# Kernel tuning notes

Hardware: AMD Instinct MI355X
Metric: run time of the kernel (lower is better)

## Reference

```python
import jax, jax.numpy as jnp
import numpy as np

N_NODES = 100_000
N_EDGES = 2_500_000
HID = 32
SE3_NORM = 1.0 / np.sqrt(32.0)  # e3nn path normalization for 32x0e -> 32x0e


def setup_inputs() -> dict:
    key = jax.random.key(0)
    ks = jax.random.split(key, 14)
    inp = {
        "pos": jax.random.normal(ks[0], (N_NODES, 3), dtype=jnp.float32),
        "edge_index": jax.random.randint(ks[1], (2, N_EDGES), 0, N_NODES, dtype=jnp.int64),
        "Wl1": jax.random.normal(ks[2], (2, HID), dtype=jnp.float32) * 0.5,
        "bl1": jax.random.normal(ks[3], (HID,), dtype=jnp.float32) * 0.1,
        "Wr1": jax.random.normal(ks[4], (2, HID), dtype=jnp.float32) * 0.5,
        "Wl2": jax.random.normal(ks[5], (HID, HID), dtype=jnp.float32) * 0.15,
        "bl2": jax.random.normal(ks[6], (HID,), dtype=jnp.float32) * 0.1,
        "Wr2": jax.random.normal(ks[7], (HID, HID), dtype=jnp.float32) * 0.15,
        "Wse1": jax.random.normal(ks[8], (HID, HID), dtype=jnp.float32) * 0.15,
        "Wse2": jax.random.normal(ks[9], (HID, HID), dtype=jnp.float32) * 0.15,
        "W3": jax.random.normal(ks[10], (HID, HID), dtype=jnp.float32) * 0.15,
        "b3": jax.random.normal(ks[11], (HID,), dtype=jnp.float32) * 0.1,
        "W4": jax.random.normal(ks[12], (HID, 1), dtype=jnp.float32) * 0.15,
        "b4": jax.random.normal(ks[13], (1,), dtype=jnp.float32) * 0.1,
        "alpha": jnp.float32(0.5),
    }
    return inp


def _sage_conv(x, src, dst, Wl, bl, Wr, n_nodes):
    # gather messages from source nodes, scatter-sum onto destination nodes
    agg = jax.ops.segment_sum(x[src], dst, num_segments=n_nodes)  # [N, d_in]
    return agg @ Wl + bl + x @ Wr  # lin_l(agg) + lin_r(x); lin_r has no bias


def reference(pos, edge_index, Wl1, bl1, Wr1, Wl2, bl2, Wr2, Wse1, Wse2, W3, b3, W4, b4, alpha):
    n = pos.shape[0]
    x = pos[:, :2]                       # [N, 2]
    src, dst = edge_index[0], edge_index[1]

    h1 = _sage_conv(x, src, dst, Wl1, bl1, Wr1, n)   # [N, 32]
    h1 = jax.nn.leaky_relu(h1, negative_slope=0.01)  # dropout = identity (eval)
    h1 = (h1 @ Wse1) * SE3_NORM                      # SE3Linear 32x0e->32x0e

    h2 = _sage_conv(h1, src, dst, Wl2, bl2, Wr2, n)
    h2 = jax.nn.leaky_relu(h2, negative_slope=0.01)
    h2 = (h2 @ Wse2) * SE3_NORM

    x_skip = alpha * h1 + h2
    x_out = jax.nn.relu(x_skip @ W3 + b3)            # mlp3 (dropout identity)
    pred = x_out @ W4 + b4                           # mlp4
    return pred.squeeze(-1)                          # [N]
```

## Files before the change

kernel.cpp:

```cpp
#include <hip/hip_runtime.h>
#include <hip/hip_fp16.h>

#define HID 32
#define LEAKY 0.01f
#define SE3NORM 0.17677669529663687f
#define SCAN_TILE 1024
#define NBK 128
#define GA 256
#define NPB2 64


__global__ void k_bhist(const int* __restrict__ ei, int* __restrict__ bh,
                        int E, int B1, int chunk) {
    extern __shared__ int lh[];
    int g = blockIdx.x;
    for (int i = threadIdx.x; i < B1; i += 256) lh[i] = 0;
    __syncthreads();
    int beg = g * chunk, end = min(E, beg + chunk);
    for (int e = beg + (int)threadIdx.x; e < end; e += 256)
        atomicAdd(&lh[ei[E + e] >> 7], 1);
    __syncthreads();
    for (int b = threadIdx.x; b < B1; b += 256) bh[b * GA + g] = lh[b];
}

__global__ void k_scan1(int* __restrict__ data, int* __restrict__ bsum, int M) {
    __shared__ int lds[256];
    int t = threadIdx.x;
    int base = blockIdx.x * SCAN_TILE + t * 4;
    int v0 = (base + 0 < M) ? data[base + 0] : 0;
    int v1 = (base + 1 < M) ? data[base + 1] : 0;
    int v2 = (base + 2 < M) ? data[base + 2] : 0;
    int v3 = (base + 3 < M) ? data[base + 3] : 0;
    int s = v0 + v1 + v2 + v3;
    lds[t] = s;
    __syncthreads();
    for (int off = 1; off < 256; off <<= 1) {
        int x = (t >= off) ? lds[t - off] : 0;
        __syncthreads();
        lds[t] += x;
        __syncthreads();
    }
    int ex = lds[t] - s;
    if (base + 0 < M) data[base + 0] = ex;
    if (base + 1 < M) data[base + 1] = ex + v0;
    if (base + 2 < M) data[base + 2] = ex + v0 + v1;
    if (base + 3 < M) data[base + 3] = ex + v0 + v1 + v2;
    if (t == 255) bsum[blockIdx.x] = lds[255];
}

__global__ void k_scan2(int* __restrict__ bsum, int B) {
    __shared__ int lds[256];
    int t = threadIdx.x;
    int v = (t < B) ? bsum[t] : 0;
    lds[t] = v;
    __syncthreads();
    for (int off = 1; off < 256; off <<= 1) {
        int x = (t >= off) ? lds[t - off] : 0;
        __syncthreads();
        lds[t] += x;
        __syncthreads();
    }
    if (t < B) bsum[t] = lds[t] - v;
}

__global__ void k_scan3(int* __restrict__ data, const int* __restrict__ bsum,
                        int* __restrict__ cursor, int M, int N) {
    int i = blockIdx.x * blockDim.x + threadIdx.x;
    if (i >= M) return;
    int off = data[i] + bsum[i / SCAN_TILE];
    data[i] = off;
    if (cursor && i < N) cursor[i] = off;
}

__global__ void k_bscatter(const int* __restrict__ ei, const int* __restrict__ bh,
                           int* __restrict__ bucketed, int E, int B1, int chunk) {
    extern __shared__ int cur[];
    int g = blockIdx.x;
    for (int b = threadIdx.x; b < B1; b += 256) cur[b] = bh[b * GA + g];
    __syncthreads();
    int beg = g * chunk, end = min(E, beg + chunk);
    for (int e = beg + (int)threadIdx.x; e < end; e += 256) {
        int d = ei[E + e];
        int s = ei[e];
        int b = d >> 7;
        int p = atomicAdd(&cur[b], 1);
        bucketed[p] = s | ((d & (NBK - 1)) << 24);
    }
}

__global__ void k_bsort(const int* __restrict__ bh, const int* __restrict__ bucketed,
                        int* __restrict__ sorted_src, int* __restrict__ offsets,
                        int E, int N, int B1) {
    __shared__ int hist[NBK], sc[NBK], base[NBK];
    int b = blockIdx.x;
    int t = threadIdx.x;
    int bs = bh[b * GA];
    int be = (b == B1 - 1) ? E : bh[(b + 1) * GA];
    if (t < NBK) hist[t] = 0;
    __syncthreads();
    for (int e = bs + t; e < be; e += 256)
        atomicAdd(&hist[bucketed[e] >> 24], 1);
    __syncthreads();
    int v = (t < NBK) ? hist[t] : 0;
    if (t < NBK) sc[t] = v;
    __syncthreads();
    for (int off = 1; off < NBK; off <<= 1) {
        int x = (t < NBK && t >= off) ? sc[t - off] : 0;
        __syncthreads();
        if (t < NBK) sc[t] += x;
        __syncthreads();
    }
    if (t < NBK) base[t] = sc[t] - v;
    __syncthreads();
    if (t < NBK) hist[t] = base[t];
    __syncthreads();
    for (int e = bs + t; e < be; e += 256) {
        int pv = bucketed[e];
        int p = atomicAdd(&hist[pv >> 24], 1);
        sorted_src[bs + p] = pv & 0x00FFFFFF;
    }
    int node = b * NBK + t;
    if (t < NBK && node < N) offsets[node] = bs + base[t];
    if (b == B1 - 1 && t == 0) offsets[N] = E;
}

__global__ void k_hist_rank(const int* __restrict__ ei, int* __restrict__ hist,
                            int* __restrict__ rank, int E) {
    int base = (blockIdx.x * blockDim.x + threadIdx.x) * 4;
#pragma unroll
    for (int u = 0; u < 4; u++) {
        int e = base + u;
        if (e < E) rank[e] = atomicAdd(&hist[ei[E + e]], 1);
    }
}
__global__ void k_hist(const int* __restrict__ ei, int* __restrict__ hist, int E) {
    int base = (blockIdx.x * blockDim.x + threadIdx.x) * 4;
#pragma unroll
    for (int u = 0; u < 4; u++) {
        int e = base + u;
        if (e < E) atomicAdd(&hist[ei[E + e]], 1);
    }
}
__global__ void k_scatter_rank(const int* __restrict__ ei, const int* __restrict__ offsets,
                               const int* __restrict__ rank, int* __restrict__ sorted_src, int E) {
    int base = (blockIdx.x * blockDim.x + threadIdx.x) * 4;
#pragma unroll
    for (int u = 0; u < 4; u++) {
        int e = base + u;
        if (e < E) sorted_src[offsets[ei[E + e]] + rank[e]] = ei[e];
    }
}
__global__ void k_scatter_atomic(const int* __restrict__ ei, int* __restrict__ cursor,
                                 int* __restrict__ sorted_src, int E) {
    int base = (blockIdx.x * blockDim.x + threadIdx.x) * 4;
#pragma unroll
    for (int u = 0; u < 4; u++) {
        int e = base + u;
        if (e < E) {
            int p = atomicAdd(&cursor[ei[E + e]], 1);
            sorted_src[p] = ei[e];
        }
    }
}

__global__ __launch_bounds__(256, 1) void k_node1(
                        const int* __restrict__ offsets, const int* __restrict__ sorted_src,
                        const float* __restrict__ pos,
                        const float* __restrict__ Wl1, const float* __restrict__ bl1,
                        const float* __restrict__ Wr1, const float* __restrict__ Wse1,
                        __half* __restrict__ h1out, int N) {
    __shared__ float sWl1[2 * HID], sWr1[2 * HID], sbl1[HID], sWse1[HID * HID];
    __shared__ float sH[32][HID + 1];
    for (int i = threadIdx.x; i < 2 * HID; i += blockDim.x) { sWl1[i] = Wl1[i]; sWr1[i] = Wr1[i]; }
    for (int i = threadIdx.x; i < HID; i += blockDim.x) sbl1[i] = bl1[i];
    for (int i = threadIdx.x; i < HID * HID; i += blockDim.x) sWse1[i] = Wse1[i];
    __syncthreads();

    const int lt = threadIdx.x;
    const int nodeL = lt >> 3;
    const int t = lt & 7;
    const int node = blockIdx.x * 32 + nodeL;
    const bool live = node < N;

    float a0 = 0.f, a1 = 0.f;
    if (live) {
        int beg = offsets[node], end = offsets[node + 1];
        for (int e = beg + t; e < end; e += 8) {
            int s = sorted_src[e];
            a0 += pos[s * 3];
            a1 += pos[s * 3 + 1];
        }
    }
    a0 += __shfl_xor(a0, 1); a1 += __shfl_xor(a1, 1);
    a0 += __shfl_xor(a0, 2); a1 += __shfl_xor(a1, 2);
    a0 += __shfl_xor(a0, 4); a1 += __shfl_xor(a1, 4);

    if (live) {
        float x0 = pos[3 * node], x1 = pos[3 * node + 1];
#pragma unroll
        for (int jj = 0; jj < 4; jj++) {
            int k = t * 4 + jj;
            float v = a0 * sWl1[k] + a1 * sWl1[HID + k] + sbl1[k] + x0 * sWr1[k] + x1 * sWr1[HID + k];
            sH[nodeL][k] = v > 0.f ? v : LEAKY * v;
        }
    }
    __syncthreads();

    if (live) {
        union Pack4 { __half h[4]; float2 v; };
        Pack4 p;
#pragma unroll
        for (int jj = 0; jj < 4; jj++) {
            int j = t * 4 + jj;
            float acc = 0.f;
#pragma unroll 8
            for (int k = 0; k < HID; k++) acc += sH[nodeL][k] * sWse1[k * HID + j];
            p.h[jj] = __float2half(acc * SE3NORM);
        }
        *(float2*)&h1out[(size_t)node * HID + t * 4] = p.v;
    }
}

__device__ __forceinline__ void acc_h1frag(float2 r, float4& acc) {
    __half2 p01 = __builtin_bit_cast(__half2, r.x);
    __half2 p23 = __builtin_bit_cast(__half2, r.y);
    acc.x += __low2float(p01); acc.y += __high2float(p01);
    acc.z += __low2float(p23); acc.w += __high2float(p23);
}

__global__ __launch_bounds__(512, 1) void k_node2out(
                           const int* __restrict__ offsets, const int* __restrict__ sorted_src,
                           const __half* __restrict__ h1,
                           const float* __restrict__ Wl2, const float* __restrict__ bl2,
                           const float* __restrict__ Wr2, const float* __restrict__ Wse2,
                           const float* __restrict__ W3, const float* __restrict__ b3,
                           const float* __restrict__ W4, const float* __restrict__ b4,
                           const float* __restrict__ alpha_p,
                           float* __restrict__ out, int N) {
    __shared__ float sWl2[HID * HID], sWr2[HID * HID], sWse2[HID * HID], sW3[HID * HID];
    __shared__ float sbl2[HID], sb3[HID], sW4[HID];
    __shared__ float sb4, salpha;
    __shared__ float sA[NPB2][HID + 1], sB[NPB2][HID + 1];
    for (int i = threadIdx.x; i < HID * HID; i += blockDim.x) {
        sWl2[i] = Wl2[i]; sWr2[i] = Wr2[i]; sWse2[i] = Wse2[i]; sW3[i] = W3[i];
    }
    for (int i = threadIdx.x; i < HID; i += blockDim.x) { sbl2[i] = bl2[i]; sb3[i] = b3[i]; sW4[i] = W4[i]; }
    if (threadIdx.x == 0) { sb4 = b4[0]; salpha = alpha_p[0]; }
    __syncthreads();

    const int lt = threadIdx.x;
    const int nodeL = lt >> 3;
    const int t = lt & 7;
    const int node = blockIdx.x * NPB2 + nodeL;
    const bool live = node < N;

    if (live) {
        float2 ro = *(const float2*)&h1[(size_t)node * HID + t * 4];

        int beg = offsets[node], end = offsets[node + 1];
        float4 acc = make_float4(0.f, 0.f, 0.f, 0.f);
        int e = beg;
        for (; e + 8 <= end; e += 8) {
            int s0 = sorted_src[e + 0], s1 = sorted_src[e + 1];
            int s2 = sorted_src[e + 2], s3 = sorted_src[e + 3];
            int s4 = sorted_src[e + 4], s5 = sorted_src[e + 5];
            int s6 = sorted_src[e + 6], s7 = sorted_src[e + 7];
            float2 r0 = *(const float2*)&h1[(size_t)s0 * HID + t * 4];
            float2 r1 = *(const float2*)&h1[(size_t)s1 * HID + t * 4];
            float2 r2 = *(const float2*)&h1[(size_t)s2 * HID + t * 4];
            float2 r3 = *(const float2*)&h1[(size_t)s3 * HID + t * 4];
            float2 r4 = *(const float2*)&h1[(size_t)s4 * HID + t * 4];
            float2 r5 = *(const float2*)&h1[(size_t)s5 * HID + t * 4];
            float2 r6 = *(const float2*)&h1[(size_t)s6 * HID + t * 4];
            float2 r7 = *(const float2*)&h1[(size_t)s7 * HID + t * 4];
            acc_h1frag(r0, acc); acc_h1frag(r1, acc);
            acc_h1frag(r2, acc); acc_h1frag(r3, acc);
            acc_h1frag(r4, acc); acc_h1frag(r5, acc);
            acc_h1frag(r6, acc); acc_h1frag(r7, acc);
        }
        for (; e + 4 <= end; e += 4) {
            int s0 = sorted_src[e + 0], s1 = sorted_src[e + 1];
            int s2 = sorted_src[e + 2], s3 = sorted_src[e + 3];
            float2 r0 = *(const float2*)&h1[(size_t)s0 * HID + t * 4];
            float2 r1 = *(const float2*)&h1[(size_t)s1 * HID + t * 4];
            float2 r2 = *(const float2*)&h1[(size_t)s2 * HID + t * 4];
            float2 r3 = *(const float2*)&h1[(size_t)s3 * HID + t * 4];
            acc_h1frag(r0, acc); acc_h1frag(r1, acc);
            acc_h1frag(r2, acc); acc_h1frag(r3, acc);
        }
        for (; e < end; e++) {
            int s = sorted_src[e];
            float2 r = *(const float2*)&h1[(size_t)s * HID + t * 4];
            acc_h1frag(r, acc);
        }
        __half2 o01 = __builtin_bit_cast(__half2, ro.x);
        __half2 o23 = __builtin_bit_cast(__half2, ro.y);
        sA[nodeL][t * 4 + 0] = acc.x; sA[nodeL][t * 4 + 1] = acc.y;
        sA[nodeL][t * 4 + 2] = acc.z; sA[nodeL][t * 4 + 3] = acc.w;
        sB[nodeL][t * 4 + 0] = __low2float(o01); sB[nodeL][t * 4 + 1] = __high2float(o01);
        sB[nodeL][t * 4 + 2] = __low2float(o23); sB[nodeL][t * 4 + 3] = __high2float(o23);
    }
    __syncthreads();

    float h2r[4];
    if (live) {
#pragma unroll
        for (int jj = 0; jj < 4; jj++) {
            int j = t * 4 + jj;
            float acc = sbl2[j];
#pragma unroll 8
            for (int k = 0; k < HID; k++)
                acc += sA[nodeL][k] * sWl2[k * HID + j] + sB[nodeL][k] * sWr2[k * HID + j];
            h2r[jj] = acc > 0.f ? acc : LEAKY * acc;
        }
    }
    __syncthreads();
    if (live) {
#pragma unroll
        for (int jj = 0; jj < 4; jj++) sA[nodeL][t * 4 + jj] = h2r[jj];
    }
    __syncthreads();

    if (live) {
#pragma unroll
        for (int jj = 0; jj < 4; jj++) {
            int j = t * 4 + jj;
            float acc = 0.f;
#pragma unroll 8
            for (int k = 0; k < HID; k++) acc += sA[nodeL][k] * sWse2[k * HID + j];
            sB[nodeL][j] = salpha * sB[nodeL][j] + acc * SE3NORM;
        }
    }
    __syncthreads();

    float part = 0.f;
#pragma unroll
    for (int jj = 0; jj < 4; jj++) {
        int j = t * 4 + jj;
        float acc = sb3[j];
        if (live) {
#pragma unroll 8
            for (int k = 0; k < HID; k++) acc += sB[nodeL][k] * sW3[k * HID + j];
        }
        part += (acc > 0.f ? acc : 0.f) * sW4[j];
    }
    part += __shfl_xor(part, 1);
    part += __shfl_xor(part, 2);
    part += __shfl_xor(part, 4);
    if (live && t == 0) out[node] = part + sb4;
}

extern "C" void kernel_launch(void* const* d_in, const int* in_sizes, int n_in,
                              void* d_out, int out_size, void* d_ws, size_t ws_size,
                              hipStream_t stream) {
    const float* pos  = (const float*)d_in[0];
    const int*   ei   = (const int*)d_in[1];
    const float* Wl1  = (const float*)d_in[2];
    const float* bl1  = (const float*)d_in[3];
    const float* Wr1  = (const float*)d_in[4];
    const float* Wl2  = (const float*)d_in[5];
    const float* bl2  = (const float*)d_in[6];
    const float* Wr2  = (const float*)d_in[7];
    const float* Wse1 = (const float*)d_in[8];
    const float* Wse2 = (const float*)d_in[9];
    const float* W3   = (const float*)d_in[10];
    const float* b3   = (const float*)d_in[11];
    const float* W4   = (const float*)d_in[12];
    const float* b4   = (const float*)d_in[13];
    const float* alp  = (const float*)d_in[14];
    float* out = (float*)d_out;

    const int N = in_sizes[0] / 3;
    const int E = in_sizes[1] / 2;
    const int blk = 256;
    const size_t h1bytes = (size_t)N * HID * sizeof(__half);

    const int B1 = (N + NBK - 1) / NBK;
    const int M2 = B1 * GA;
    const int S2 = (M2 + SCAN_TILE - 1) / SCAN_TILE;
    {
        int* bh         = (int*)d_ws;
        int* bsum       = bh + M2;
        int* bucketed   = bsum + 256;
        int* sorted_src = bucketed + E;
        int* offsets    = sorted_src + E;
        uintptr_t hp = ((uintptr_t)(offsets + N + 1) + 15) & ~(uintptr_t)15;
        size_t need = (hp - (uintptr_t)d_ws) + h1bytes;
        if (need <= ws_size && S2 <= 256) {
            __half* h1 = (__half*)hp;
            const int chunk = (E + GA - 1) / GA;
            const size_t ldsB = (size_t)B1 * sizeof(int);
            k_bhist<<<GA, 256, ldsB, stream>>>(ei, bh, E, B1, chunk);
            k_scan1<<<S2, 256, 0, stream>>>(bh, bsum, M2);
            k_scan2<<<1, 256, 0, stream>>>(bsum, S2);
            k_scan3<<<(M2 + blk - 1) / blk, blk, 0, stream>>>(bh, bsum, nullptr, M2, 0);
            k_bscatter<<<GA, 256, ldsB, stream>>>(ei, bh, bucketed, E, B1, chunk);
            k_bsort<<<B1, 256, 0, stream>>>(bh, bucketed, sorted_src, offsets, E, N, B1);
            k_node1<<<(N + 31) / 32, 256, 0, stream>>>(offsets, sorted_src, pos,
                                                       Wl1, bl1, Wr1, Wse1, h1, N);
            k_node2out<<<(N + NPB2 - 1) / NPB2, 512, 0, stream>>>(offsets, sorted_src, h1,
                                                          Wl2, bl2, Wr2, Wse2,
                                                          W3, b3, W4, b4, alp, out, N);
            return;
        }
    }

    const int M = N + 1;
    const int B = (M + SCAN_TILE - 1) / SCAN_TILE;
    int* hist       = (int*)d_ws;
    int* offsets    = hist + M;
    int* bsum       = offsets + M;
    int* sorted_src = bsum + 256;
    int* aux        = sorted_src + E;
    uintptr_t hpA = ((uintptr_t)(aux + E) + 15) & ~(uintptr_t)15;
    uintptr_t hpB = ((uintptr_t)(aux + N) + 15) & ~(uintptr_t)15;
    size_t needA = (hpA - (uintptr_t)d_ws) + h1bytes;
    const bool useRank = (needA <= ws_size);
    __half* h1 = (__half*)(useRank ? hpA : hpB);

    hipMemsetAsync(hist, 0, (size_t)M * sizeof(int), stream);
    const int egrid4 = (E / 4 + blk) / blk;
    if (useRank) {
        k_hist_rank<<<egrid4, blk, 0, stream>>>(ei, hist, aux, E);
    } else {
        k_hist<<<egrid4, blk, 0, stream>>>(ei, hist, E);
    }
    k_scan1<<<B, 256, 0, stream>>>(hist, bsum, M);
    k_scan2<<<1, 256, 0, stream>>>(bsum, B);
    k_scan3<<<(M + blk - 1) / blk, blk, 0, stream>>>(hist, bsum, useRank ? nullptr : aux, M, N);
    int* offs = hist;
    if (useRank) {
        k_scatter_rank<<<egrid4, blk, 0, stream>>>(ei, offs, aux, sorted_src, E);
    } else {
        k_scatter_atomic<<<egrid4, blk, 0, stream>>>(ei, aux, sorted_src, E);
    }
    k_node1<<<(N + 31) / 32, 256, 0, stream>>>(offs, sorted_src, pos, Wl1, bl1, Wr1, Wse1, h1, N);
    k_node2out<<<(N + NPB2 - 1) / NPB2, 512, 0, stream>>>(offs, sorted_src, h1, Wl2, bl2, Wr2, Wse2,
                                                  W3, b3, W4, b4, alp, out, N);
}
```

Baseline: 258.8 us.

## Split h1 into two half-width planes and vectorize small matmuls with float4

Stores the fp16 h1 features as two separate 16-channel planes (32 bytes per node each), so the layer-2 gather runs in two passes, each touching a smaller, more cache-friendly array. Each thread now loads 4 bytes per neighbour per pass instead of 8 bytes once. The per-node 32x32 matmuls are rewritten to read weights as float4 from LDS, with padding changed to HID+4 for alignment. The cost is reading the edge list twice and issuing twice as many gather instructions.

```diff
diff --git a/kernel.cpp b/kernel.cpp
--- a/kernel.cpp
+++ b/kernel.cpp
@@ -168,9 +168,9 @@
                         const float* __restrict__ pos,
                         const float* __restrict__ Wl1, const float* __restrict__ bl1,
                         const float* __restrict__ Wr1, const float* __restrict__ Wse1,
-                        __half* __restrict__ h1out, int N) {
+                        __half* __restrict__ h1a, __half* __restrict__ h1b, int N) {
     __shared__ float sWl1[2 * HID], sWr1[2 * HID], sbl1[HID], sWse1[HID * HID];
-    __shared__ float sH[32][HID + 1];
+    __shared__ float sH[32][HID + 4];
     for (int i = threadIdx.x; i < 2 * HID; i += blockDim.x) { sWl1[i] = Wl1[i]; sWr1[i] = Wr1[i]; }
     for (int i = threadIdx.x; i < HID; i += blockDim.x) sbl1[i] = bl1[i];
     for (int i = threadIdx.x; i < HID * HID; i += blockDim.x) sWse1[i] = Wse1[i];
@@ -207,30 +207,33 @@
     __syncthreads();
 
     if (live) {
+        float4 acc = make_float4(0.f, 0.f, 0.f, 0.f);
+#pragma unroll 8
+        for (int k = 0; k < HID; k++) {
+            float hk = sH[nodeL][k];
+            float4 w = *(const float4*)&sWse1[k * HID + t * 4];
+            acc.x += hk * w.x; acc.y += hk * w.y;
+            acc.z += hk * w.z; acc.w += hk * w.w;
+        }
         union Pack4 { __half h[4]; float2 v; };
         Pack4 p;
-#pragma unroll
-        for (int jj = 0; jj < 4; jj++) {
-            int j = t * 4 + jj;
-            float acc = 0.f;
-#pragma unroll 8
-            for (int k = 0; k < HID; k++) acc += sH[nodeL][k] * sWse1[k * HID + j];
-            p.h[jj] = __float2half(acc * SE3NORM);
-        }
-        *(float2*)&h1out[(size_t)node * HID + t * 4] = p.v;
-    }
-}
-
-__device__ __forceinline__ void acc_h1frag(float2 r, float4& acc) {
-    __half2 p01 = __builtin_bit_cast(__half2, r.x);
-    __half2 p23 = __builtin_bit_cast(__half2, r.y);
-    acc.x += __low2float(p01); acc.y += __high2float(p01);
-    acc.z += __low2float(p23); acc.w += __high2float(p23);
+        p.h[0] = __float2half(acc.x * SE3NORM);
+        p.h[1] = __float2half(acc.y * SE3NORM);
+        p.h[2] = __float2half(acc.z * SE3NORM);
+        p.h[3] = __float2half(acc.w * SE3NORM);
+        if (t < 4) *(float2*)&h1a[(size_t)node * 16 + t * 4] = p.v;
+        else       *(float2*)&h1b[(size_t)node * 16 + (t - 4) * 4] = p.v;
+    }
+}
+
+__device__ __forceinline__ void acc_pair(unsigned int r, float& x, float& y) {
+    __half2 p = __builtin_bit_cast(__half2, r);
+    x += __low2float(p); y += __high2float(p);
 }
 
 __global__ __launch_bounds__(512, 1) void k_node2out(
                            const int* __restrict__ offsets, const int* __restrict__ sorted_src,
-                           const __half* __restrict__ h1,
+                           const __half* __restrict__ h1a, const __half* __restrict__ h1b,
                            const float* __restrict__ Wl2, const float* __restrict__ bl2,
                            const float* __restrict__ Wr2, const float* __restrict__ Wse2,
                            const float* __restrict__ W3, const float* __restrict__ b3,
@@ -240,7 +243,7 @@
     __shared__ float sWl2[HID * HID], sWr2[HID * HID], sWse2[HID * HID], sW3[HID * HID];
     __shared__ float sbl2[HID], sb3[HID], sW4[HID];
     __shared__ float sb4, salpha;
-    __shared__ float sA[NPB2][HID + 1], sB[NPB2][HID + 1];
+    __shared__ float sA[NPB2][HID + 4], sB[NPB2][HID + 4];
     for (int i = threadIdx.x; i < HID * HID; i += blockDim.x) {
         sWl2[i] = Wl2[i]; sWr2[i] = Wr2[i]; sWse2[i] = Wse2[i]; sW3[i] = W3[i];
     }
@@ -255,95 +258,132 @@
     const bool live = node < N;
 
     if (live) {
-        float2 ro = *(const float2*)&h1[(size_t)node * HID + t * 4];
-
-        int beg = offsets[node], end = offsets[node + 1];
-        float4 acc = make_float4(0.f, 0.f, 0.f, 0.f);
+        const int beg = offsets[node], end = offsets[node + 1];
+        unsigned int oa = *(const unsigned int*)((const char*)h1a + ((size_t)node * 32 + t * 4));
+        unsigned int ob = *(const unsigned int*)((const char*)h1b + ((size_t)node * 32 + t * 4));
+
+        float a0 = 0.f, a1 = 0.f;
         int e = beg;
         for (; e + 8 <= end; e += 8) {
             int s0 = sorted_src[e + 0], s1 = sorted_src[e + 1];
             int s2 = sorted_src[e + 2], s3 = sorted_src[e + 3];
             int s4 = sorted_src[e + 4], s5 = sorted_src[e + 5];
             int s6 = sorted_src[e + 6], s7 = sorted_src[e + 7];
-            float2 r0 = *(const float2*)&h1[(size_t)s0 * HID + t * 4];
-            float2 r1 = *(const float2*)&h1[(size_t)s1 * HID + t * 4];
-            float2 r2 = *(const float2*)&h1[(size_t)s2 * HID + t * 4];
-            float2 r3 = *(const float2*)&h1[(size_t)s3 * HID + t * 4];
-            float2 r4 = *(const float2*)&h1[(size_t)s4 * HID + t * 4];
-            float2 r5 = *(const float2*)&h1[(size_t)s5 * HID + t * 4];
-            float2 r6 = *(const float2*)&h1[(size_t)s6 * HID + t * 4];
-            float2 r7 = *(const float2*)&h1[(size_t)s7 * HID + t * 4];
-            acc_h1frag(r0, acc); acc_h1frag(r1, acc);
-            acc_h1frag(r2, acc); acc_h1frag(r3, acc);
-            acc_h1frag(r4, acc); acc_h1frag(r5, acc);
-            acc_h1frag(r6, acc); acc_h1frag(r7, acc);
-        }
-        for (; e + 4 <= end; e += 4) {
+            unsigned int r0 = *(const unsigned int*)((const char*)h1a + ((size_t)s0 * 32 + t * 4));
+            unsigned int r1 = *(const unsigned int*)((const char*)h1a + ((size_t)s1 * 32 + t * 4));
+            unsigned int r2 = *(const unsigned int*)((const char*)h1a + ((size_t)s2 * 32 + t * 4));
+            unsigned int r3 = *(const unsigned int*)((const char*)h1a + ((size_t)s3 * 32 + t * 4));
+            unsigned int r4 = *(const unsigned int*)((const char*)h1a + ((size_t)s4 * 32 + t * 4));
+            unsigned int r5 = *(const unsigned int*)((const char*)h1a + ((size_t)s5 * 32 + t * 4));
+            unsigned int r6 = *(const unsigned int*)((const char*)h1a + ((size_t)s6 * 32 + t * 4));
+            unsigned int r7 = *(const unsigned int*)((const char*)h1a + ((size_t)s7 * 32 + t * 4));
+            acc_pair(r0, a0, a1); acc_pair(r1, a0, a1);
+            acc_pair(r2, a0, a1); acc_pair(r3, a0, a1);
+            acc_pair(r4, a0, a1); acc_pair(r5, a0, a1);
+            acc_pair(r6, a0, a1); acc_pair(r7, a0, a1);
+        }
+        for (; e < end; e++) {
+            int s = sorted_src[e];
+            unsigned int r = *(const unsigned int*)((const char*)h1a + ((size_t)s * 32 + t * 4));
+            acc_pair(r, a0, a1);
+        }
+        sA[nodeL][t * 2 + 0] = a0;
+        sA[nodeL][t * 2 + 1] = a1;
+
+        float b0 = 0.f, b1 = 0.f;
+        e = beg;
+        for (; e + 8 <= end; e += 8) {
             int s0 = sorted_src[e + 0], s1 = sorted_src[e + 1];
             int s2 = sorted_src[e + 2], s3 = sorted_src[e + 3];
-            float2 r0 = *(const float2*)&h1[(size_t)s0 * HID + t * 4];
-            float2 r1 = *(const float2*)&h1[(size_t)s1 * HID + t * 4];
-            float2 r2 = *(const float2*)&h1[(size_t)s2 * HID + t * 4];
-            float2 r3 = *(const float2*)&h1[(size_t)s3 * HID + t * 4];
-            acc_h1frag(r0, acc); acc_h1frag(r1, acc);
-            acc_h1frag(r2, acc); acc_h1frag(r3, acc);
+            int s4 = sorted_src[e + 4], s5 = sorted_src[e + 5];
+            int s6 = sorted_src[e + 6], s7 = sorted_src[e + 7];
+            unsigned int r0 = *(const unsigned int*)((const char*)h1b + ((size_t)s0 * 32 + t * 4));
+            unsigned int r1 = *(const unsigned int*)((const char*)h1b + ((size_t)s1 * 32 + t * 4));
+            unsigned int r2 = *(const unsigned int*)((const char*)h1b + ((size_t)s2 * 32 + t * 4));
+            unsigned int r3 = *(const unsigned int*)((const char*)h1b + ((size_t)s3 * 32 + t * 4));
+            unsigned int r4 = *(const unsigned int*)((const char*)h1b + ((size_t)s4 * 32 + t * 4));
+            unsigned int r5 = *(const unsigned int*)((const char*)h1b + ((size_t)s5 * 32 + t * 4));
+            unsigned int r6 = *(const unsigned int*)((const char*)h1b + ((size_t)s6 * 32 + t * 4));
+            unsigned int r7 = *(const unsigned int*)((const char*)h1b + ((size_t)s7 * 32 + t * 4));
+            acc_pair(r0, b0, b1); acc_pair(r1, b0, b1);
+            acc_pair(r2, b0, b1); acc_pair(r3, b0, b1);
+            acc_pair(r4, b0, b1); acc_pair(r5, b0, b1);
+            acc_pair(r6, b0, b1); acc_pair(r7, b0, b1);
         }
         for (; e < end; e++) {
             int s = sorted_src[e];
-            float2 r = *(const float2*)&h1[(size_t)s * HID + t * 4];
-            acc_h1frag(r, acc);
-        }
-        __half2 o01 = __builtin_bit_cast(__half2, ro.x);
-        __half2 o23 = __builtin_bit_cast(__half2, ro.y);
-        sA[nodeL][t * 4 + 0] = acc.x; sA[nodeL][t * 4 + 1] = acc.y;
-        sA[nodeL][t * 4 + 2] = acc.z; sA[nodeL][t * 4 + 3] = acc.w;
-        sB[nodeL][t * 4 + 0] = __low2float(o01); sB[nodeL][t * 4 + 1] = __high2float(o01);
-        sB[nodeL][t * 4 + 2] = __low2float(o23); sB[nodeL][t * 4 + 3] = __high2float(o23);
+            unsigned int r = *(const unsigned int*)((const char*)h1b + ((size_t)s * 32 + t * 4));
+            acc_pair(r, b0, b1);
+        }
+        sA[nodeL][16 + t * 2 + 0] = b0;
+        sA[nodeL][16 + t * 2 + 1] = b1;
+
+        __half2 pa = __builtin_bit_cast(__half2, oa);
+        __half2 pb = __builtin_bit_cast(__half2, ob);
+        sB[nodeL][t * 2 + 0]      = __low2float(pa); sB[nodeL][t * 2 + 1]      = __high2float(pa);
+        sB[nodeL][16 + t * 2 + 0] = __low2float(pb); sB[nodeL][16 + t * 2 + 1] = __high2float(pb);
     }
     __syncthreads();
 
     float h2r[4];
     if (live) {
-#pragma unroll
-        for (int jj = 0; jj < 4; jj++) {
-            int j = t * 4 + jj;
-            float acc = sbl2[j];
+        h2r[0] = sbl2[t * 4 + 0]; h2r[1] = sbl2[t * 4 + 1];
+        h2r[2] = sbl2[t * 4 + 2]; h2r[3] = sbl2[t * 4 + 3];
 #pragma unroll 8
-            for (int k = 0; k < HID; k++)
-                acc += sA[nodeL][k] * sWl2[k * HID + j] + sB[nodeL][k] * sWr2[k * HID + j];
-            h2r[jj] = acc > 0.f ? acc : LEAKY * acc;
-        }
-    }
-    __syncthreads();
-    if (live) {
-#pragma unroll
-        for (int jj = 0; jj < 4; jj++) sA[nodeL][t * 4 + jj] = h2r[jj];
-    }
-    __syncthreads();
-
-    if (live) {
-#pragma unroll
-        for (int jj = 0; jj < 4; jj++) {
-            int j = t * 4 + jj;
-            float acc = 0.f;
+        for (int k = 0; k < HID; k++) {
+            float a = sA[nodeL][k];
+            float b = sB[nodeL][k];
+            float4 wl = *(const float4*)&sWl2[k * HID + t * 4];
+            float4 wr = *(const float4*)&sWr2[k * HID + t * 4];
+            h2r[0] += a * wl.x + b * wr.x;
+            h2r[1] += a * wl.y + b * wr.y;
+            h2r[2] += a * wl.z + b * wr.z;
+            h2r[3] += a * wl.w + b * wr.w;
+        }
+#pragma unroll
+        for (int jj = 0; jj < 4; jj++) h2r[jj] = h2r[jj] > 0.f ? h2r[jj] : LEAKY * h2r[jj];
+    }
+    __syncthreads();
+    if (live) {
+        float4 st = make_float4(h2r[0], h2r[1], h2r[2], h2r[3]);
+        *(float4*)&sA[nodeL][t * 4] = st;
+    }
+    __syncthreads();
+
+    if (live) {
+        float4 acc = make_float4(0.f, 0.f, 0.f, 0.f);
 #pragma unroll 8
-            for (int k = 0; k < HID; k++) acc += sA[nodeL][k] * sWse2[k * HID + j];
-            sB[nodeL][j] = salpha * sB[nodeL][j] + acc * SE3NORM;
-        }
-    }
-    __syncthreads();
-
+        for (int k = 0; k < HID; k++) {
+            float a = sA[nodeL][k];
+            float4 w = *(const float4*)&sWse2[k * HID + t * 4];
+            acc.x += a * w.x; acc.y += a * w.y;
+            acc.z += a * w.z; acc.w += a * w.w;
+        }
+        float4 own = *(const float4*)&sB[nodeL][t * 4];
+        own.x = salpha * own.x + acc.x * SE3NORM;
+        own.y = salpha * own.y + acc.y * SE3NORM;
+        own.z = salpha * own.z + acc.z * SE3NORM;
+        own.w = salpha * own.w + acc.w * SE3NORM;
+        *(float4*)&sB[nodeL][t * 4] = own;
+    }
+    __syncthreads();
+
+    float acc4[4];
+    acc4[0] = sb3[t * 4 + 0]; acc4[1] = sb3[t * 4 + 1];
+    acc4[2] = sb3[t * 4 + 2]; acc4[3] = sb3[t * 4 + 3];
+    if (live) {
+#pragma unroll 8
+        for (int k = 0; k < HID; k++) {
+            float s = sB[nodeL][k];
+            float4 w = *(const float4*)&sW3[k * HID + t * 4];
+            acc4[0] += s * w.x; acc4[1] += s * w.y;
+            acc4[2] += s * w.z; acc4[3] += s * w.w;
+        }
+    }
     float part = 0.f;
 #pragma unroll
-    for (int jj = 0; jj < 4; jj++) {
-        int j = t * 4 + jj;
-        float acc = sb3[j];
-        if (live) {
-#pragma unroll 8
-            for (int k = 0; k < HID; k++) acc += sB[nodeL][k] * sW3[k * HID + j];
-        }
-        part += (acc > 0.f ? acc : 0.f) * sW4[j];
-    }
+    for (int jj = 0; jj < 4; jj++)
+        part += (acc4[jj] > 0.f ? acc4[jj] : 0.f) * sW4[t * 4 + jj];
     part += __shfl_xor(part, 1);
     part += __shfl_xor(part, 2);
     part += __shfl_xor(part, 4);
@@ -387,7 +427,8 @@
         uintptr_t hp = ((uintptr_t)(offsets + N + 1) + 15) & ~(uintptr_t)15;
         size_t need = (hp - (uintptr_t)d_ws) + h1bytes;
         if (need <= ws_size && S2 <= 256) {
-            __half* h1 = (__half*)hp;
+            __half* h1a = (__half*)hp;
+            __half* h1b = h1a + (size_t)N * 16;
             const int chunk = (E + GA - 1) / GA;
             const size_t ldsB = (size_t)B1 * sizeof(int);
             k_bhist<<<GA, 256, ldsB, stream>>>(ei, bh, E, B1, chunk);
@@ -397,8 +438,8 @@
             k_bscatter<<<GA, 256, ldsB, stream>>>(ei, bh, bucketed, E, B1, chunk);
             k_bsort<<<B1, 256, 0, stream>>>(bh, bucketed, sorted_src, offsets, E, N, B1);
             k_node1<<<(N + 31) / 32, 256, 0, stream>>>(offsets, sorted_src, pos,
-                                                       Wl1, bl1, Wr1, Wse1, h1, N);
-            k_node2out<<<(N + NPB2 - 1) / NPB2, 512, 0, stream>>>(offsets, sorted_src, h1,
+                                                       Wl1, bl1, Wr1, Wse1, h1a, h1b, N);
+            k_node2out<<<(N + NPB2 - 1) / NPB2, 512, 0, stream>>>(offsets, sorted_src, h1a, h1b,
                                                           Wl2, bl2, Wr2, Wse2,
                                                           W3, b3, W4, b4, alp, out, N);
             return;
@@ -416,7 +457,8 @@
     uintptr_t hpB = ((uintptr_t)(aux + N) + 15) & ~(uintptr_t)15;
     size_t needA = (hpA - (uintptr_t)d_ws) + h1bytes;
     const bool useRank = (needA <= ws_size);
-    __half* h1 = (__half*)(useRank ? hpA : hpB);
+    __half* h1a = (__half*)(useRank ? hpA : hpB);
+    __half* h1b = h1a + (size_t)N * 16;
 
     hipMemsetAsync(hist, 0, (size_t)M * sizeof(int), stream);
     const int egrid4 = (E / 4 + blk) / blk;
@@ -434,7 +476,7 @@
     } else {
         k_scatter_atomic<<<egrid4, blk, 0, stream>>>(ei, aux, sorted_src, E);
     }
-    k_node1<<<(N + 31) / 32, 256, 0, stream>>>(offs, sorted_src, pos, Wl1, bl1, Wr1, Wse1, h1, N);
-    k_node2out<<<(N + NPB2 - 1) / NPB2, 512, 0, stream>>>(offs, sorted_src, h1, Wl2, bl2, Wr2, Wse2,
+    k_node1<<<(N + 31) / 32, 256, 0, stream>>>(offs, sorted_src, pos, Wl1, bl1, Wr1, Wse1, h1a, h1b, N);
+    k_node2out<<<(N + NPB2 - 1) / NPB2, 512, 0, stream>>>(offs, sorted_src, h1a, h1b, Wl2, bl2, Wr2, Wse2,
                                                   W3, b3, W4, b4, alp, out, N);
 }
```

Measured after the change: 257.8 us. No clear change (-0.4%).

## Fuse bucket sort with layer-1 node computation and vectorize LDS matvecs

Applied to the files above, without the earlier changes.

Merges the per-bucket sort kernel with the first SAGE layer. While counting destination histograms, the block accumulates pos[src] x/y sums into shared atomics, then computes h1 for its 128 nodes in the same block. This removes one launch and the second pass over sorted_src. The change also adds nontemporal loads on edge streams, float4 weight reads from LDS with +4 padding in the matvecs, and drops the 4-wide tail loop. Float shared atomics make the summation order nondeterministic, and each block has only 128 destination nodes of work for layer 1.

```diff
diff --git a/kernel.cpp b/kernel.cpp
--- a/kernel.cpp
+++ b/kernel.cpp
@@ -18,7 +18,7 @@
     __syncthreads();
     int beg = g * chunk, end = min(E, beg + chunk);
     for (int e = beg + (int)threadIdx.x; e < end; e += 256)
-        atomicAdd(&lh[ei[E + e] >> 7], 1);
+        atomicAdd(&lh[__builtin_nontemporal_load(&ei[E + e]) >> 7], 1);
     __syncthreads();
     for (int b = threadIdx.x; b < B1; b += 256) bh[b * GA + g] = lh[b];
 }
@@ -80,26 +80,42 @@
     __syncthreads();
     int beg = g * chunk, end = min(E, beg + chunk);
     for (int e = beg + (int)threadIdx.x; e < end; e += 256) {
-        int d = ei[E + e];
-        int s = ei[e];
+        int d = __builtin_nontemporal_load(&ei[E + e]);
+        int s = __builtin_nontemporal_load(&ei[e]);
         int b = d >> 7;
         int p = atomicAdd(&cur[b], 1);
         bucketed[p] = s | ((d & (NBK - 1)) << 24);
     }
 }
 
-__global__ void k_bsort(const int* __restrict__ bh, const int* __restrict__ bucketed,
-                        int* __restrict__ sorted_src, int* __restrict__ offsets,
-                        int E, int N, int B1) {
+__global__ __launch_bounds__(256, 1) void k_bsort_node1(
+        const int* __restrict__ bh, const int* __restrict__ bucketed,
+        const float* __restrict__ pos,
+        const float* __restrict__ Wl1, const float* __restrict__ bl1,
+        const float* __restrict__ Wr1, const float* __restrict__ Wse1,
+        int* __restrict__ sorted_src, int* __restrict__ offsets,
+        __half* __restrict__ h1, int E, int N, int B1) {
     __shared__ int hist[NBK], sc[NBK], base[NBK];
-    int b = blockIdx.x;
-    int t = threadIdx.x;
-    int bs = bh[b * GA];
-    int be = (b == B1 - 1) ? E : bh[(b + 1) * GA];
-    if (t < NBK) hist[t] = 0;
-    __syncthreads();
-    for (int e = bs + t; e < be; e += 256)
-        atomicAdd(&hist[bucketed[e] >> 24], 1);
+    __shared__ float aggx[NBK], aggy[NBK];
+    __shared__ float sWl1[2 * HID], sWr1[2 * HID], sbl1[HID], sWse1[HID * HID];
+    __shared__ float sH[32][HID + 4];
+    const int b = blockIdx.x;
+    const int t = threadIdx.x;
+    for (int i = t; i < 2 * HID; i += 256) { sWl1[i] = Wl1[i]; sWr1[i] = Wr1[i]; }
+    for (int i = t; i < HID; i += 256) sbl1[i] = bl1[i];
+    for (int i = t; i < HID * HID; i += 256) sWse1[i] = Wse1[i];
+    const int bs = bh[b * GA];
+    const int be = (b == B1 - 1) ? E : bh[(b + 1) * GA];
+    if (t < NBK) { hist[t] = 0; aggx[t] = 0.f; aggy[t] = 0.f; }
+    __syncthreads();
+    for (int e = bs + t; e < be; e += 256) {
+        int pv = bucketed[e];
+        int dl = pv >> 24;
+        int s = pv & 0x00FFFFFF;
+        atomicAdd(&hist[dl], 1);
+        atomicAdd(&aggx[dl], pos[s * 3]);
+        atomicAdd(&aggy[dl], pos[s * 3 + 1]);
+    }
     __syncthreads();
     int v = (t < NBK) ? hist[t] : 0;
     if (t < NBK) sc[t] = v;
@@ -119,9 +135,46 @@
         int p = atomicAdd(&hist[pv >> 24], 1);
         sorted_src[bs + p] = pv & 0x00FFFFFF;
     }
-    int node = b * NBK + t;
-    if (t < NBK && node < N) offsets[node] = bs + base[t];
+    int nodeg = b * NBK + t;
+    if (t < NBK && nodeg < N) offsets[nodeg] = bs + base[t];
     if (b == B1 - 1 && t == 0) offsets[N] = E;
+    __syncthreads();
+    const int nodeL = t >> 3;
+    const int lane = t & 7;
+    for (int c = 0; c < NBK / 32; c++) {
+        const int dl = c * 32 + nodeL;
+        const int node = b * NBK + dl;
+        const bool live = node < N;
+        if (live) {
+            float a0 = aggx[dl], a1 = aggy[dl];
+            float x0 = pos[3 * node], x1 = pos[3 * node + 1];
+#pragma unroll
+            for (int jj = 0; jj < 4; jj++) {
+                int k = lane * 4 + jj;
+                float vv = a0 * sWl1[k] + a1 * sWl1[HID + k] + sbl1[k]
+                         + x0 * sWr1[k] + x1 * sWr1[HID + k];
+                sH[nodeL][k] = vv > 0.f ? vv : LEAKY * vv;
+            }
+        }
+        __syncthreads();
+        if (live) {
+            float4 acc = make_float4(0.f, 0.f, 0.f, 0.f);
+#pragma unroll 8
+            for (int k = 0; k < HID; k++) {
+                float hk = sH[nodeL][k];
+                float4 w = *(const float4*)&sWse1[k * HID + lane * 4];
+                acc.x += hk * w.x; acc.y += hk * w.y;
+                acc.z += hk * w.z; acc.w += hk * w.w;
+            }
+            union Pack4 { __half h[4]; float2 v; } p;
+            p.h[0] = __float2half(acc.x * SE3NORM);
+            p.h[1] = __float2half(acc.y * SE3NORM);
+            p.h[2] = __float2half(acc.z * SE3NORM);
+            p.h[3] = __float2half(acc.w * SE3NORM);
+            *(float2*)&h1[(size_t)node * HID + lane * 4] = p.v;
+        }
+        __syncthreads();
+    }
 }
 
 __global__ void k_hist_rank(const int* __restrict__ ei, int* __restrict__ hist,
@@ -168,9 +221,9 @@
                         const float* __restrict__ pos,
                         const float* __restrict__ Wl1, const float* __restrict__ bl1,
                         const float* __restrict__ Wr1, const float* __restrict__ Wse1,
-                        __half* __restrict__ h1out, int N) {
+                        __half* __restrict__ h1, int N) {
     __shared__ float sWl1[2 * HID], sWr1[2 * HID], sbl1[HID], sWse1[HID * HID];
-    __shared__ float sH[32][HID + 1];
+    __shared__ float sH[32][HID + 4];
     for (int i = threadIdx.x; i < 2 * HID; i += blockDim.x) { sWl1[i] = Wl1[i]; sWr1[i] = Wr1[i]; }
     for (int i = threadIdx.x; i < HID; i += blockDim.x) sbl1[i] = bl1[i];
     for (int i = threadIdx.x; i < HID * HID; i += blockDim.x) sWse1[i] = Wse1[i];
@@ -207,17 +260,20 @@
     __syncthreads();
 
     if (live) {
-        union Pack4 { __half h[4]; float2 v; };
-        Pack4 p;
-#pragma unroll
-        for (int jj = 0; jj < 4; jj++) {
-            int j = t * 4 + jj;
-            float acc = 0.f;
+        float4 acc = make_float4(0.f, 0.f, 0.f, 0.f);
 #pragma unroll 8
-            for (int k = 0; k < HID; k++) acc += sH[nodeL][k] * sWse1[k * HID + j];
-            p.h[jj] = __float2half(acc * SE3NORM);
-        }
-        *(float2*)&h1out[(size_t)node * HID + t * 4] = p.v;
+        for (int k = 0; k < HID; k++) {
+            float hk = sH[nodeL][k];
+            float4 w = *(const float4*)&sWse1[k * HID + t * 4];
+            acc.x += hk * w.x; acc.y += hk * w.y;
+            acc.z += hk * w.z; acc.w += hk * w.w;
+        }
+        union Pack4 { __half h[4]; float2 v; } p;
+        p.h[0] = __float2half(acc.x * SE3NORM);
+        p.h[1] = __float2half(acc.y * SE3NORM);
+        p.h[2] = __float2half(acc.z * SE3NORM);
+        p.h[3] = __float2half(acc.w * SE3NORM);
+        *(float2*)&h1[(size_t)node * HID + t * 4] = p.v;
     }
 }
 
@@ -240,7 +296,7 @@
     __shared__ float sWl2[HID * HID], sWr2[HID * HID], sWse2[HID * HID], sW3[HID * HID];
     __shared__ float sbl2[HID], sb3[HID], sW4[HID];
     __shared__ float sb4, salpha;
-    __shared__ float sA[NPB2][HID + 1], sB[NPB2][HID + 1];
+    __shared__ float sA[NPB2][HID + 4], sB[NPB2][HID + 4];
     for (int i = threadIdx.x; i < HID * HID; i += blockDim.x) {
         sWl2[i] = Wl2[i]; sWr2[i] = Wr2[i]; sWse2[i] = Wse2[i]; sW3[i] = W3[i];
     }
@@ -261,10 +317,14 @@
         float4 acc = make_float4(0.f, 0.f, 0.f, 0.f);
         int e = beg;
         for (; e + 8 <= end; e += 8) {
-            int s0 = sorted_src[e + 0], s1 = sorted_src[e + 1];
-            int s2 = sorted_src[e + 2], s3 = sorted_src[e + 3];
-            int s4 = sorted_src[e + 4], s5 = sorted_src[e + 5];
-            int s6 = sorted_src[e + 6], s7 = sorted_src[e + 7];
+            int s0 = __builtin_nontemporal_load(&sorted_src[e + 0]);
+            int s1 = __builtin_nontemporal_load(&sorted_src[e + 1]);
+            int s2 = __builtin_nontemporal_load(&sorted_src[e + 2]);
+            int s3 = __builtin_nontemporal_load(&sorted_src[e + 3]);
+            int s4 = __builtin_nontemporal_load(&sorted_src[e + 4]);
+            int s5 = __builtin_nontemporal_load(&sorted_src[e + 5]);
+            int s6 = __builtin_nontemporal_load(&sorted_src[e + 6]);
+            int s7 = __builtin_nontemporal_load(&sorted_src[e + 7]);
             float2 r0 = *(const float2*)&h1[(size_t)s0 * HID + t * 4];
             float2 r1 = *(const float2*)&h1[(size_t)s1 * HID + t * 4];
             float2 r2 = *(const float2*)&h1[(size_t)s2 * HID + t * 4];
@@ -278,72 +338,79 @@
             acc_h1frag(r4, acc); acc_h1frag(r5, acc);
             acc_h1frag(r6, acc); acc_h1frag(r7, acc);
         }
-        for (; e + 4 <= end; e += 4) {
-            int s0 = sorted_src[e + 0], s1 = sorted_src[e + 1];
-            int s2 = sorted_src[e + 2], s3 = sorted_src[e + 3];
-            float2 r0 = *(const float2*)&h1[(size_t)s0 * HID + t * 4];
-            float2 r1 = *(const float2*)&h1[(size_t)s1 * HID + t * 4];
-            float2 r2 = *(const float2*)&h1[(size_t)s2 * HID + t * 4];
-            float2 r3 = *(const float2*)&h1[(size_t)s3 * HID + t * 4];
-            acc_h1frag(r0, acc); acc_h1frag(r1, acc);
-            acc_h1frag(r2, acc); acc_h1frag(r3, acc);
-        }
         for (; e < end; e++) {
-            int s = sorted_src[e];
+            int s = __builtin_nontemporal_load(&sorted_src[e]);
             float2 r = *(const float2*)&h1[(size_t)s * HID + t * 4];
             acc_h1frag(r, acc);
         }
         __half2 o01 = __builtin_bit_cast(__half2, ro.x);
         __half2 o23 = __builtin_bit_cast(__half2, ro.y);
-        sA[nodeL][t * 4 + 0] = acc.x; sA[nodeL][t * 4 + 1] = acc.y;
-        sA[nodeL][t * 4 + 2] = acc.z; sA[nodeL][t * 4 + 3] = acc.w;
-        sB[nodeL][t * 4 + 0] = __low2float(o01); sB[nodeL][t * 4 + 1] = __high2float(o01);
-        sB[nodeL][t * 4 + 2] = __low2float(o23); sB[nodeL][t * 4 + 3] = __high2float(o23);
+        float4 own = make_float4(__low2float(o01), __high2float(o01),
+                                 __low2float(o23), __high2float(o23));
+        *(float4*)&sA[nodeL][t * 4] = acc;
+        *(float4*)&sB[nodeL][t * 4] = own;
     }
     __syncthreads();
 
     float h2r[4];
     if (live) {
-#pragma unroll
-        for (int jj = 0; jj < 4; jj++) {
-            int j = t * 4 + jj;
-            float acc = sbl2[j];
+        h2r[0] = sbl2[t * 4 + 0]; h2r[1] = sbl2[t * 4 + 1];
+        h2r[2] = sbl2[t * 4 + 2]; h2r[3] = sbl2[t * 4 + 3];
 #pragma unroll 8
-            for (int k = 0; k < HID; k++)
-                acc += sA[nodeL][k] * sWl2[k * HID + j] + sB[nodeL][k] * sWr2[k * HID + j];
-            h2r[jj] = acc > 0.f ? acc : LEAKY * acc;
-        }
-    }
-    __syncthreads();
-    if (live) {
-#pragma unroll
-        for (int jj = 0; jj < 4; jj++) sA[nodeL][t * 4 + jj] = h2r[jj];
-    }
-    __syncthreads();
-
-    if (live) {
-#pragma unroll
-        for (int jj = 0; jj < 4; jj++) {
-            int j = t * 4 + jj;
-            float acc = 0.f;
+        for (int k = 0; k < HID; k++) {
+            float a = sA[nodeL][k];
+            float b = sB[nodeL][k];
+            float4 wl = *(const float4*)&sWl2[k * HID + t * 4];
+            float4 wr = *(const float4*)&sWr2[k * HID + t * 4];
+            h2r[0] += a * wl.x + b * wr.x;
+            h2r[1] += a * wl.y + b * wr.y;
+            h2r[2] += a * wl.z + b * wr.z;
+            h2r[3] += a * wl.w + b * wr.w;
+        }
+#pragma unroll
+        for (int jj = 0; jj < 4; jj++) h2r[jj] = h2r[jj] > 0.f ? h2r[jj] : LEAKY * h2r[jj];
+    }
+    __syncthreads();
+    if (live) {
+        float4 st = make_float4(h2r[0], h2r[1], h2r[2], h2r[3]);
+        *(float4*)&sA[nodeL][t * 4] = st;
+    }
+    __syncthreads();
+
+    if (live) {
+        float4 acc = make_float4(0.f, 0.f, 0.f, 0.f);
 #pragma unroll 8
-            for (int k = 0; k < HID; k++) acc += sA[nodeL][k] * sWse2[k * HID + j];
-            sB[nodeL][j] = salpha * sB[nodeL][j] + acc * SE3NORM;
-        }
-    }
-    __syncthreads();
-
+        for (int k = 0; k < HID; k++) {
+            float a = sA[nodeL][k];
+            float4 w = *(const float4*)&sWse2[k * HID + t * 4];
+            acc.x += a * w.x; acc.y += a * w.y;
+            acc.z += a * w.z; acc.w += a * w.w;
+        }
+        float4 own = *(const float4*)&sB[nodeL][t * 4];
+        own.x = salpha * own.x + acc.x * SE3NORM;
+        own.y = salpha * own.y + acc.y * SE3NORM;
+        own.z = salpha * own.z + acc.z * SE3NORM;
+        own.w = salpha * own.w + acc.w * SE3NORM;
+        *(float4*)&sB[nodeL][t * 4] = own;
+    }
+    __syncthreads();
+
+    float acc4[4];
+    acc4[0] = sb3[t * 4 + 0]; acc4[1] = sb3[t * 4 + 1];
+    acc4[2] = sb3[t * 4 + 2]; acc4[3] = sb3[t * 4 + 3];
+    if (live) {
+#pragma unroll 8
+        for (int k = 0; k < HID; k++) {
+            float s = sB[nodeL][k];
+            float4 w = *(const float4*)&sW3[k * HID + t * 4];
+            acc4[0] += s * w.x; acc4[1] += s * w.y;
+            acc4[2] += s * w.z; acc4[3] += s * w.w;
+        }
+    }
     float part = 0.f;
 #pragma unroll
-    for (int jj = 0; jj < 4; jj++) {
-        int j = t * 4 + jj;
-        float acc = sb3[j];
-        if (live) {
-#pragma unroll 8
-            for (int k = 0; k < HID; k++) acc += sB[nodeL][k] * sW3[k * HID + j];
-        }
-        part += (acc > 0.f ? acc : 0.f) * sW4[j];
-    }
+    for (int jj = 0; jj < 4; jj++)
+        part += (acc4[jj] > 0.f ? acc4[jj] : 0.f) * sW4[t * 4 + jj];
     part += __shfl_xor(part, 1);
     part += __shfl_xor(part, 2);
     part += __shfl_xor(part, 4);
@@ -395,9 +462,9 @@
             k_scan2<<<1, 256, 0, stream>>>(bsum, S2);
             k_scan3<<<(M2 + blk - 1) / blk, blk, 0, stream>>>(bh, bsum, nullptr, M2, 0);
             k_bscatter<<<GA, 256, ldsB, stream>>>(ei, bh, bucketed, E, B1, chunk);
-            k_bsort<<<B1, 256, 0, stream>>>(bh, bucketed, sorted_src, offsets, E, N, B1);
-            k_node1<<<(N + 31) / 32, 256, 0, stream>>>(offsets, sorted_src, pos,
-                                                       Wl1, bl1, Wr1, Wse1, h1, N);
+            k_bsort_node1<<<B1, 256, 0, stream>>>(bh, bucketed, pos,
+                                                  Wl1, bl1, Wr1, Wse1,
+                                                  sorted_src, offsets, h1, E, N, B1);
             k_node2out<<<(N + NPB2 - 1) / NPB2, 512, 0, stream>>>(offsets, sorted_src, h1,
                                                           Wl2, bl2, Wr2, Wse2,
                                                           W3, b3, W4, b4, alp, out, N);
```

New measurement: 281.8 us. 8.9% more time.
